# Performance work log

Measured on AMD Instinct MI355X. Metric: run time of the kernel, lower is better.

Reference implementation:

```python
import jax, jax.numpy as jnp
import numpy as np

N_NODES = 50000
N_EDGES = 800000
IN_DIM, HID, OUT = 512, 96, 64


def gcn_conv(x, W, b, src, dst, n_nodes):
    # PyG GCNConv: h = x W; aggregate with sym-normalized adjacency incl. self-loops; add bias.
    h = x @ W  # [N, out]
    ones = jnp.ones_like(dst, dtype=h.dtype)
    deg = jax.ops.segment_sum(ones, dst, num_segments=n_nodes) + 1.0  # +1 for self-loop
    dinv = jax.lax.rsqrt(deg)
    norm = dinv[src] * dinv[dst]  # [E]
    agg = jax.ops.segment_sum(h[src] * norm[:, None], dst, num_segments=n_nodes)
    agg = agg + h * (dinv * dinv)[:, None]  # self-loop messages
    return agg + b


def setup_inputs() -> dict:
    key = jax.random.key(0)
    ks = jax.random.split(key, 12)
    s = 0.05
    x = jax.random.normal(ks[0], (N_NODES, IN_DIM), jnp.float32)
    edge_index = jax.random.randint(ks[1], (2, N_EDGES), 0, N_NODES)
    return {
        "x": x,
        "edge_index": edge_index,
        "W0": jax.random.normal(ks[2], (IN_DIM, HID), jnp.float32) * s,
        "b0": jnp.zeros((HID,), jnp.float32),
        "W1": jax.random.normal(ks[3], (HID, HID), jnp.float32) * s,
        "b1": jnp.zeros((HID,), jnp.float32),
        "W2": jax.random.normal(ks[4], (HID, HID), jnp.float32) * s,
        "b2": jnp.zeros((HID,), jnp.float32),
        "fcW": jax.random.normal(ks[5], (HID, OUT), jnp.float32) * s,
        "fcb": jnp.zeros((OUT,), jnp.float32),
    }


def reference(x, edge_index, W0, b0, W1, b1, W2, b2, fcW, fcb):
    src, dst = edge_index[0], edge_index[1]
    n = x.shape[0]
    # eval mode: dropout is identity; bn=False so no batchnorm
    h = jax.nn.relu(gcn_conv(x, W0, b0, src, dst, n))
    h = jax.nn.relu(gcn_conv(h, W1, b1, src, dst, n))
    h = jax.nn.relu(gcn_conv(h, W2, b2, src, dst, n))
    out = h @ fcW + fcb
    return jnp.squeeze(out)
```

## Files before the change

kernel.cpp:

```cpp
#include <hip/hip_runtime.h>


constexpr int NN   = 50000;
constexpr int NE   = 800000;
constexpr int KIN  = 512;
constexpr int HIDD = 96;
constexpr int ODIM = 64;
constexpr int NBLK = (NN + 255) / 256;

typedef short bf16x8 __attribute__((ext_vector_type(8)));
typedef float f32x4  __attribute__((ext_vector_type(4)));
typedef _Float16 h4  __attribute__((ext_vector_type(4)));

__device__ inline short f2bf(float f) {
    union { float f; unsigned u; } v; v.f = f;
    unsigned r = v.u + 0x7FFFu + ((v.u >> 16) & 1u);
    return (short)(r >> 16);
}
__device__ inline short f2bf_trunc(float f) {
    union { float f; unsigned u; } v; v.f = f;
    return (short)(v.u >> 16);
}
__device__ inline float bf2f(short h) {
    union { unsigned u; float f; } v; v.u = ((unsigned)(unsigned short)h) << 16;
    return v.f;
}

__global__ void zero_int_kernel(int* __restrict__ p, int n) {
    int i = blockIdx.x * blockDim.x + threadIdx.x;
    if (i < n) p[i] = 0;
}

__global__ void hist_kernel(const int* __restrict__ dst, int* __restrict__ deg) {
    int e = blockIdx.x * blockDim.x + threadIdx.x;
    if (e < NE) atomicAdd(&deg[dst[e]], 1);
}

__global__ void scan1_kernel(const int* __restrict__ deg, int* __restrict__ excl,
                             int* __restrict__ partials) {
    __shared__ int tmp[256];
    const int tid = threadIdx.x;
    const int i = blockIdx.x * 256 + tid;
    const int v = (i < NN) ? deg[i] : 0;
    tmp[tid] = v;
    __syncthreads();
#pragma unroll
    for (int off = 1; off < 256; off <<= 1) {
        int t = (tid >= off) ? tmp[tid - off] : 0;
        __syncthreads();
        tmp[tid] += t;
        __syncthreads();
    }
    if (i < NN) excl[i] = tmp[tid] - v;
    if (tid == 255) partials[blockIdx.x] = tmp[tid];
}

__global__ void scan3_kernel(const int* __restrict__ excl, const int* __restrict__ partials,
                             const int* __restrict__ deg, int* __restrict__ rowstart,
                             float* __restrict__ dinv, int* __restrict__ cursor) {
    __shared__ int tmp[256];
    const int tid = threadIdx.x;
    tmp[tid] = (tid < (int)blockIdx.x) ? partials[tid] : 0;
    __syncthreads();
#pragma unroll
    for (int off = 128; off > 0; off >>= 1) {
        if (tid < off) tmp[tid] += tmp[tid + off];
        __syncthreads();
    }
    const int boff = tmp[0];
    const int i = blockIdx.x * 256 + tid;
    if (i < NN) {
        rowstart[i] = excl[i] + boff;
        dinv[i] = 1.0f / sqrtf((float)deg[i] + 1.0f);
        cursor[i] = 0;
    }
}

__global__ void scatter_kernel(const int* __restrict__ src, const int* __restrict__ dst,
                               const int* __restrict__ rowstart, int* __restrict__ cursor,
                               int* __restrict__ csr_src) {
    int e = blockIdx.x * blockDim.x + threadIdx.x;
    if (e < NE) {
        const int d = dst[e];
        const int pos = rowstart[d] + atomicAdd(&cursor[d], 1);
        csr_src[pos] = src[e];
    }
}

__global__ void pack_all(const float* __restrict__ W0, const float* __restrict__ W1,
                         const float* __restrict__ W2, const float* __restrict__ FC,
                         short* __restrict__ w0hi, short* __restrict__ w0lo,
                         short* __restrict__ w1hi, short* __restrict__ w1lo,
                         short* __restrict__ w2hi, short* __restrict__ w2lo,
                         short* __restrict__ fchi, short* __restrict__ fclo) {
    const int idx = blockIdx.x * 256 + threadIdx.x;
    const float* W; short *hi, *lo; int M, li;
    if      (idx < 49152) { W = W0; hi = w0hi; lo = w0lo; M = 96; li = idx; }
    else if (idx < 58368) { W = W1; hi = w1hi; lo = w1lo; M = 96; li = idx - 49152; }
    else if (idx < 67584) { W = W2; hi = w2hi; lo = w2lo; M = 96; li = idx - 58368; }
    else if (idx < 73728) { W = FC; hi = fchi; lo = fclo; M = 64; li = idx - 67584; }
    else return;
    const int CT = M >> 4;
    const int j = li & 7;
    const int lane = (li >> 3) & 63;
    const int t = li >> 9;
    const int ct = t % CT;
    const int kc = t / CT;
    const int k = kc * 32 + (lane >> 4) * 8 + j;
    const int n = ct * 16 + (lane & 15);
    const float w = W[k * M + n];
    const short h = f2bf(w);
    hi[li] = h;
    lo[li] = f2bf_trunc(w - bf2f(h));
}

template <int K>
__launch_bounds__(512, 6)
__global__ void mfma_gemm_f(const float* __restrict__ A, const short* __restrict__ Whi,
                            const short* __restrict__ Wlo, const float* __restrict__ dinv,
                            _Float16* __restrict__ C, int N) {
    constexpr int CT = 6;
    constexpr int KCH = K / 64;
    constexpr int PH  = KCH / 2;
    __shared__ short sHi[4 * 3072];
    __shared__ short sLo[4 * 3072];

    const int tid = threadIdx.x;
    const int lane = tid & 63;
    const int wave = tid >> 6;
    const int rw = wave & 3;
    const int kh = wave >> 2;
    const int q = lane >> 4;
    const int m = lane & 15;
    const int row = blockIdx.x * 64 + rw * 16 + m;
    const int arow = (row < N) ? row : (N - 1);

    f32x4 acc[CT];
#pragma unroll
    for (int c = 0; c < CT; ++c) acc[c] = f32x4{0.f, 0.f, 0.f, 0.f};

    const float* ap = A + (size_t)arow * K + kh * (K / 2) + q * 8;
    float4 a0 = *(const float4*)(ap);
    float4 a1 = *(const float4*)(ap + 4);

#pragma unroll
    for (int p = 0; p < PH; ++p) {
#pragma unroll
        for (int i = 0; i < 3; ++i) {
            const int ci = i * 512 + tid;
            const int slot = ci / 384;
            const int within = ci - slot * 384;
            const int kcg = (slot >> 1) * KCH + p * 2 + (slot & 1);
            const int so = kcg * 3072 + within * 8;
            const int doff = ci * 8;
            *(float4*)(sHi + doff) = *(const float4*)(Whi + so);
            *(float4*)(sLo + doff) = *(const float4*)(Wlo + so);
        }
        __syncthreads();

#pragma unroll
        for (int kc = 0; kc < 2; ++kc) {
            const float af[8] = {a0.x, a0.y, a0.z, a0.w, a1.x, a1.y, a1.z, a1.w};
            bf16x8 ahi, alo;
#pragma unroll
            for (int j = 0; j < 8; ++j) {
                const short h = f2bf(af[j]);
                ahi[j] = h;
                alo[j] = f2bf_trunc(af[j] - bf2f(h));
            }
            if (p * 2 + kc + 1 < KCH) {
                ap += 32;
                a0 = *(const float4*)(ap);
                a1 = *(const float4*)(ap + 4);
            }
            const int slot = kh * 2 + kc;
            const short* hbase = sHi + slot * 3072 + lane * 8;
            const short* lbase = sLo + slot * 3072 + lane * 8;
#pragma unroll
            for (int c = 0; c < CT; ++c) {
                const bf16x8 wh = *(const bf16x8*)(hbase + c * 512);
                const bf16x8 wl = *(const bf16x8*)(lbase + c * 512);
                acc[c] = __builtin_amdgcn_mfma_f32_16x16x32_bf16(ahi, wh, acc[c], 0, 0, 0);
                acc[c] = __builtin_amdgcn_mfma_f32_16x16x32_bf16(alo, wh, acc[c], 0, 0, 0);
                acc[c] = __builtin_amdgcn_mfma_f32_16x16x32_bf16(ahi, wl, acc[c], 0, 0, 0);
            }
        }
        __syncthreads();
    }

    float* sAcc = (float*)sHi;
    if (kh == 1) {
#pragma unroll
        for (int c = 0; c < CT; ++c)
            *(f32x4*)(sAcc + ((rw * 64 + lane) * CT + c) * 4) = acc[c];
    }
    __syncthreads();
    if (kh == 0) {
#pragma unroll
        for (int c = 0; c < CT; ++c) {
            const f32x4 o = *(const f32x4*)(sAcc + ((rw * 64 + lane) * CT + c) * 4);
            acc[c][0] += o[0]; acc[c][1] += o[1]; acc[c][2] += o[2]; acc[c][3] += o[3];
        }
        const int rbase = blockIdx.x * 64 + rw * 16 + q * 4;
#pragma unroll
        for (int r = 0; r < 4; ++r) {
            const int orow = rbase + r;
            if (orow < N) {
                const float s = dinv[orow];
#pragma unroll
                for (int c = 0; c < CT; ++c)
                    C[(size_t)orow * 96 + c * 16 + m] = (_Float16)(acc[c][r] * s);
            }
        }
    }
}

constexpr int APAD = 104;
template <int M, bool FC>
__launch_bounds__(512, 6)
__global__ void fused_gg(const int* __restrict__ rowstart, const int* __restrict__ deg,
                         const int* __restrict__ csr_src, const float* __restrict__ dinv,
                         const h4* __restrict__ hs, const float* __restrict__ gb,
                         const short* __restrict__ Whi, const short* __restrict__ Wlo,
                         const float* __restrict__ bias2,
                         _Float16* __restrict__ Ch, float* __restrict__ Cf, int N) {
    constexpr int CT = M / 16;
    constexpr int CTH = CT / 2;
    __shared__ short sAhi[64 * APAD];
    __shared__ short sAlo[64 * APAD];

    const int tid = threadIdx.x;
    const int nl = tid >> 3;
    const int f8 = tid & 7;
    const int node = blockIdx.x * 64 + nl;
    const bool valid = node < N;

    float acc[12];
#pragma unroll
    for (int i = 0; i < 12; ++i) acc[i] = 0.0f;

    if (valid) {
        const h4* __restrict__ hp = hs + (size_t)node * 24 + f8 * 3;
        {
            const h4 s0 = hp[0], s1 = hp[1], s2 = hp[2];
#pragma unroll
            for (int e = 0; e < 4; ++e) {
                acc[e] += (float)s0[e]; acc[4 + e] += (float)s1[e]; acc[8 + e] += (float)s2[e];
            }
        }
        int j = rowstart[node];
        const int jend = j + deg[node];
        for (; j + 4 <= jend; j += 4) {
            int s[4];
#pragma unroll
            for (int i = 0; i < 4; ++i) s[i] = csr_src[j + i];
            h4 v[4][3];
#pragma unroll
            for (int i = 0; i < 4; ++i) {
                const h4* __restrict__ p = hs + (size_t)s[i] * 24 + f8 * 3;
                v[i][0] = p[0]; v[i][1] = p[1]; v[i][2] = p[2];
            }
#pragma unroll
            for (int i = 0; i < 4; ++i)
#pragma unroll
                for (int e = 0; e < 4; ++e) {
                    acc[e] += (float)v[i][0][e];
                    acc[4 + e] += (float)v[i][1][e];
                    acc[8 + e] += (float)v[i][2][e];
                }
        }
        for (; j < jend; ++j) {
            const h4* __restrict__ p = hs + (size_t)csr_src[j] * 24 + f8 * 3;
            const h4 v0 = p[0], v1 = p[1], v2 = p[2];
#pragma unroll
            for (int e = 0; e < 4; ++e) {
                acc[e] += (float)v0[e]; acc[4 + e] += (float)v1[e]; acc[8 + e] += (float)v2[e];
            }
        }
        const float di = dinv[node];
        short4 hi[3], lo[3];
#pragma unroll
        for (int t = 0; t < 3; ++t) {
#pragma unroll
            for (int e = 0; e < 4; ++e) {
                const float o = fmaxf(fmaf(di, acc[t * 4 + e], gb[f8 * 12 + t * 4 + e]), 0.0f);
                const short h = f2bf(o);
                ((short*)&hi[t])[e] = h;
                ((short*)&lo[t])[e] = f2bf_trunc(o - bf2f(h));
            }
        }
        short* dh = sAhi + nl * APAD + f8 * 12;
        short* dl = sAlo + nl * APAD + f8 * 12;
#pragma unroll
        for (int t = 0; t < 3; ++t) {
            *(short4*)(dh + t * 4) = hi[t];
            *(short4*)(dl + t * 4) = lo[t];
        }
    } else {
        short* dh = sAhi + nl * APAD + f8 * 12;
        short* dl = sAlo + nl * APAD + f8 * 12;
        const short4 z = {0, 0, 0, 0};
#pragma unroll
        for (int t = 0; t < 3; ++t) { *(short4*)(dh + t * 4) = z; *(short4*)(dl + t * 4) = z; }
    }
    __syncthreads();

    const int lane = tid & 63;
    const int wave = tid >> 6;
    const int rw = wave & 3;
    const int c0 = (wave >> 2) * CTH;
    const int q = lane >> 4;
    const int m = lane & 15;

    bf16x8 Ah[3], Al[3];
#pragma unroll
    for (int kc = 0; kc < 3; ++kc) {
        const int off = (rw * 16 + m) * APAD + kc * 32 + q * 8;
        Ah[kc] = *(const bf16x8*)(sAhi + off);
        Al[kc] = *(const bf16x8*)(sAlo + off);
    }

    f32x4 gacc[CTH];
#pragma unroll
    for (int c = 0; c < CTH; ++c) gacc[c] = f32x4{0.f, 0.f, 0.f, 0.f};

#pragma unroll
    for (int kc = 0; kc < 3; ++kc) {
#pragma unroll
        for (int c = 0; c < CTH; ++c) {
            const int fo = ((kc * CT + c0 + c) * 64 + lane) * 8;
            const bf16x8 wh = *(const bf16x8*)(Whi + fo);
            const bf16x8 wl = *(const bf16x8*)(Wlo + fo);
            gacc[c] = __builtin_amdgcn_mfma_f32_16x16x32_bf16(Ah[kc], wh, gacc[c], 0, 0, 0);
            gacc[c] = __builtin_amdgcn_mfma_f32_16x16x32_bf16(Al[kc], wh, gacc[c], 0, 0, 0);
            gacc[c] = __builtin_amdgcn_mfma_f32_16x16x32_bf16(Ah[kc], wl, gacc[c], 0, 0, 0);
        }
    }

    const int rbase = blockIdx.x * 64 + rw * 16 + q * 4;
#pragma unroll
    for (int r = 0; r < 4; ++r) {
        const int orow = rbase + r;
        if (orow < N) {
            if (FC) {
#pragma unroll
                for (int c = 0; c < CTH; ++c)
                    Cf[(size_t)orow * M + (c0 + c) * 16 + m] = gacc[c][r] + bias2[(c0 + c) * 16 + m];
            } else {
                const float s = dinv[orow];
#pragma unroll
                for (int c = 0; c < CTH; ++c)
                    Ch[(size_t)orow * M + (c0 + c) * 16 + m] = (_Float16)(gacc[c][r] * s);
            }
        }
    }
}

extern "C" void kernel_launch(void* const* d_in, const int* in_sizes, int n_in,
                              void* d_out, int out_size, void* d_ws, size_t ws_size,
                              hipStream_t stream) {
    const float* x   = (const float*)d_in[0];
    const int*   ei  = (const int*)d_in[1];
    const float* W0  = (const float*)d_in[2];
    const float* b0  = (const float*)d_in[3];
    const float* W1  = (const float*)d_in[4];
    const float* b1  = (const float*)d_in[5];
    const float* W2  = (const float*)d_in[6];
    const float* b2  = (const float*)d_in[7];
    const float* fcW = (const float*)d_in[8];
    const float* fcb = (const float*)d_in[9];
    float* out = (float*)d_out;

    const int* src = ei;
    const int* dst = ei + NE;

    float* ws = (float*)d_ws;
    float* dinv     = ws;
    int*   deg      = (int*)(ws + 50176);
    int*   excl     = (int*)(ws + 100352);
    int*   cursor   = (int*)(ws + 150528);
    int*   rowstart = (int*)(ws + 200704);
    int*   partials = (int*)(ws + 250880);
    int*   csr_src  = (int*)(ws + 251136);
    short* w0hi = (short*)(ws + 1051392);
    short* w0lo = (short*)(ws + 1075968);
    short* w1hi = (short*)(ws + 1100544);
    short* w1lo = (short*)(ws + 1105152);
    short* w2hi = (short*)(ws + 1109760);
    short* w2lo = (short*)(ws + 1114368);
    short* fchi = (short*)(ws + 1118976);
    short* fclo = (short*)(ws + 1122048);
    _Float16* hsA = (_Float16*)(ws + 1125120);
    _Float16* hsB = (_Float16*)(ws + 3525120);

    dim3 b256(256);
    const int gN = NBLK;
    const int gE = (NE + 255) / 256;
    const int gGem = (NN + 63) / 64;
    const int gPack = (73728 + 255) / 256;

    zero_int_kernel<<<gN, b256, 0, stream>>>(deg, NN);
    hist_kernel<<<gE, b256, 0, stream>>>(dst, deg);
    scan1_kernel<<<gN, b256, 0, stream>>>(deg, excl, partials);
    scan3_kernel<<<gN, b256, 0, stream>>>(excl, partials, deg, rowstart, dinv, cursor);
    scatter_kernel<<<gE, b256, 0, stream>>>(src, dst, rowstart, cursor, csr_src);
    pack_all<<<gPack, b256, 0, stream>>>(W0, W1, W2, fcW, w0hi, w0lo, w1hi, w1lo,
                                         w2hi, w2lo, fchi, fclo);

    mfma_gemm_f<KIN><<<gGem, dim3(512), 0, stream>>>(x, w0hi, w0lo, dinv, hsA, NN);

    fused_gg<HIDD, false><<<gGem, dim3(512), 0, stream>>>(
        rowstart, deg, csr_src, dinv, (const h4*)hsA, b0, w1hi, w1lo, nullptr, hsB, nullptr, NN);

    fused_gg<HIDD, false><<<gGem, dim3(512), 0, stream>>>(
        rowstart, deg, csr_src, dinv, (const h4*)hsB, b1, w2hi, w2lo, nullptr, hsA, nullptr, NN);

    fused_gg<ODIM, true><<<gGem, dim3(512), 0, stream>>>(
        rowstart, deg, csr_src, dinv, (const h4*)hsA, b2, fchi, fclo, fcb, nullptr, out, NN);
}
```

Before: 377.8 us.

## Balance edge aggregation across threads with merge-path split and LDS atomics

Each block's edge range is now split evenly across its 64 thread groups instead of one group per node. Each group accumulates runs of edges that share a destination and flushes them into a shared-memory accumulator with atomics. The local destination index is packed into the high bits of the CSR source entries, and rowstart gets a sentinel entry. This aims to remove load imbalance from varying node degrees, at the cost of LDS atomics, an extra zeroing pass and extra barriers.

```diff
diff --git a/kernel.cpp b/kernel.cpp
--- a/kernel.cpp
+++ b/kernel.cpp
@@ -74,6 +74,7 @@
         dinv[i] = 1.0f / sqrtf((float)deg[i] + 1.0f);
         cursor[i] = 0;
     }
+    if (blockIdx.x == 0 && tid == 0) rowstart[NN] = NE;
 }
 
 __global__ void scatter_kernel(const int* __restrict__ src, const int* __restrict__ dst,
@@ -83,7 +84,7 @@
     if (e < NE) {
         const int d = dst[e];
         const int pos = rowstart[d] + atomicAdd(&cursor[d], 1);
-        csr_src[pos] = src[e];
+        csr_src[pos] = src[e] | ((d & 63) << 20);
     }
 }
 
@@ -216,92 +217,106 @@
 }
 
 constexpr int APAD = 104;
+constexpr int ACCS = 97;
 template <int M, bool FC>
 __launch_bounds__(512, 6)
-__global__ void fused_gg(const int* __restrict__ rowstart, const int* __restrict__ deg,
-                         const int* __restrict__ csr_src, const float* __restrict__ dinv,
-                         const h4* __restrict__ hs, const float* __restrict__ gb,
+__global__ void fused_gg(const int* __restrict__ rowstart, const float* __restrict__ dinv,
+                         const int* __restrict__ csr_src, const h4* __restrict__ hs,
+                         const float* __restrict__ gb,
                          const short* __restrict__ Whi, const short* __restrict__ Wlo,
                          const float* __restrict__ bias2,
                          _Float16* __restrict__ Ch, float* __restrict__ Cf, int N) {
     constexpr int CT = M / 16;
     constexpr int CTH = CT / 2;
-    __shared__ short sAhi[64 * APAD];
-    __shared__ short sAlo[64 * APAD];
+    __shared__ short SMEM[2 * 64 * APAD];
+    float* accf = (float*)SMEM;
+    short* sAhi = SMEM;
+    short* sAlo = SMEM + 64 * APAD;
 
     const int tid = threadIdx.x;
+    const int nb = blockIdx.x * 64;
+
+    for (int i = tid; i < 64 * ACCS; i += 512) accf[i] = 0.0f;
+    __syncthreads();
+
+    {
+        const int e0 = rowstart[nb];
+        const int top = (nb + 64 < N) ? nb + 64 : N;
+        const int T = rowstart[top] - e0;
+        const int g = tid >> 3;
+        const int f8 = tid & 7;
+        const int per = (T + 63) >> 6;
+        int j = g * per;
+        const int jend = (j + per < T) ? (j + per) : T;
+
+        float racc[12];
+#pragma unroll
+        for (int i = 0; i < 12; ++i) racc[i] = 0.f;
+        int curloc = -1;
+        int v = (j < jend) ? csr_src[e0 + j] : 0;
+        while (j < jend) {
+            const int vn = (j + 1 < jend) ? csr_src[e0 + j + 1] : 0;
+            const int s = v & 0xFFFFF;
+            const int loc = v >> 20;
+            if (loc != curloc) {
+                if (curloc >= 0) {
+#pragma unroll
+                    for (int i = 0; i < 12; ++i)
+                        atomicAdd(&accf[curloc * ACCS + f8 * 12 + i], racc[i]);
+                }
+#pragma unroll
+                for (int i = 0; i < 12; ++i) racc[i] = 0.f;
+                curloc = loc;
+            }
+            const h4* __restrict__ p = hs + (size_t)s * 24 + f8 * 3;
+            const h4 p0 = p[0], p1 = p[1], p2 = p[2];
+#pragma unroll
+            for (int e = 0; e < 4; ++e) {
+                racc[e] += (float)p0[e]; racc[4 + e] += (float)p1[e]; racc[8 + e] += (float)p2[e];
+            }
+            v = vn; ++j;
+        }
+        if (curloc >= 0) {
+#pragma unroll
+            for (int i = 0; i < 12; ++i)
+                atomicAdd(&accf[curloc * ACCS + f8 * 12 + i], racc[i]);
+        }
+    }
+    __syncthreads();
+
     const int nl = tid >> 3;
-    const int f8 = tid & 7;
-    const int node = blockIdx.x * 64 + nl;
-    const bool valid = node < N;
-
-    float acc[12];
-#pragma unroll
-    for (int i = 0; i < 12; ++i) acc[i] = 0.0f;
-
-    if (valid) {
-        const h4* __restrict__ hp = hs + (size_t)node * 24 + f8 * 3;
-        {
-            const h4 s0 = hp[0], s1 = hp[1], s2 = hp[2];
-#pragma unroll
-            for (int e = 0; e < 4; ++e) {
-                acc[e] += (float)s0[e]; acc[4 + e] += (float)s1[e]; acc[8 + e] += (float)s2[e];
-            }
-        }
-        int j = rowstart[node];
-        const int jend = j + deg[node];
-        for (; j + 4 <= jend; j += 4) {
-            int s[4];
-#pragma unroll
-            for (int i = 0; i < 4; ++i) s[i] = csr_src[j + i];
-            h4 v[4][3];
-#pragma unroll
-            for (int i = 0; i < 4; ++i) {
-                const h4* __restrict__ p = hs + (size_t)s[i] * 24 + f8 * 3;
-                v[i][0] = p[0]; v[i][1] = p[1]; v[i][2] = p[2];
-            }
-#pragma unroll
-            for (int i = 0; i < 4; ++i)
-#pragma unroll
-                for (int e = 0; e < 4; ++e) {
-                    acc[e] += (float)v[i][0][e];
-                    acc[4 + e] += (float)v[i][1][e];
-                    acc[8 + e] += (float)v[i][2][e];
-                }
-        }
-        for (; j < jend; ++j) {
-            const h4* __restrict__ p = hs + (size_t)csr_src[j] * 24 + f8 * 3;
-            const h4 v0 = p[0], v1 = p[1], v2 = p[2];
-#pragma unroll
-            for (int e = 0; e < 4; ++e) {
-                acc[e] += (float)v0[e]; acc[4 + e] += (float)v1[e]; acc[8 + e] += (float)v2[e];
-            }
-        }
+    const int fc8 = tid & 7;
+    const int node = nb + nl;
+    short hi[12], lo[12];
+    if (node < N) {
+        const h4* __restrict__ hp = hs + (size_t)node * 24 + fc8 * 3;
+        const h4 s0 = hp[0], s1 = hp[1], s2 = hp[2];
         const float di = dinv[node];
-        short4 hi[3], lo[3];
-#pragma unroll
-        for (int t = 0; t < 3; ++t) {
-#pragma unroll
-            for (int e = 0; e < 4; ++e) {
-                const float o = fmaxf(fmaf(di, acc[t * 4 + e], gb[f8 * 12 + t * 4 + e]), 0.0f);
-                const short h = f2bf(o);
-                ((short*)&hi[t])[e] = h;
-                ((short*)&lo[t])[e] = f2bf_trunc(o - bf2f(h));
-            }
-        }
-        short* dh = sAhi + nl * APAD + f8 * 12;
-        short* dl = sAlo + nl * APAD + f8 * 12;
-#pragma unroll
-        for (int t = 0; t < 3; ++t) {
-            *(short4*)(dh + t * 4) = hi[t];
-            *(short4*)(dl + t * 4) = lo[t];
+        float a[12];
+#pragma unroll
+        for (int i = 0; i < 12; ++i) a[i] = accf[nl * ACCS + fc8 * 12 + i];
+#pragma unroll
+        for (int e = 0; e < 4; ++e) {
+            a[e] += (float)s0[e]; a[4 + e] += (float)s1[e]; a[8 + e] += (float)s2[e];
+        }
+#pragma unroll
+        for (int i = 0; i < 12; ++i) {
+            const float o = fmaxf(fmaf(di, a[i], gb[fc8 * 12 + i]), 0.0f);
+            hi[i] = f2bf(o);
+            lo[i] = f2bf_trunc(o - bf2f(hi[i]));
         }
     } else {
-        short* dh = sAhi + nl * APAD + f8 * 12;
-        short* dl = sAlo + nl * APAD + f8 * 12;
-        const short4 z = {0, 0, 0, 0};
-#pragma unroll
-        for (int t = 0; t < 3; ++t) { *(short4*)(dh + t * 4) = z; *(short4*)(dl + t * 4) = z; }
+#pragma unroll
+        for (int i = 0; i < 12; ++i) { hi[i] = 0; lo[i] = 0; }
+    }
+    __syncthreads();
+
+    short* dh = sAhi + nl * APAD + fc8 * 12;
+    short* dl = sAlo + nl * APAD + fc8 * 12;
+#pragma unroll
+    for (int t = 0; t < 3; ++t) {
+        *(short4*)(dh + t * 4) = make_short4(hi[4 * t], hi[4 * t + 1], hi[4 * t + 2], hi[4 * t + 3]);
+        *(short4*)(dl + t * 4) = make_short4(lo[4 * t], lo[4 * t + 1], lo[4 * t + 2], lo[4 * t + 3]);
     }
     __syncthreads();
 
@@ -337,7 +352,7 @@
         }
     }
 
-    const int rbase = blockIdx.x * 64 + rw * 16 + q * 4;
+    const int rbase = nb + rw * 16 + q * 4;
 #pragma unroll
     for (int r = 0; r < 4; ++r) {
         const int orow = rbase + r;
@@ -410,11 +425,11 @@
     mfma_gemm_f<KIN><<<gGem, dim3(512), 0, stream>>>(x, w0hi, w0lo, dinv, hsA, NN);
 
     fused_gg<HIDD, false><<<gGem, dim3(512), 0, stream>>>(
-        rowstart, deg, csr_src, dinv, (const h4*)hsA, b0, w1hi, w1lo, nullptr, hsB, nullptr, NN);
+        rowstart, dinv, csr_src, (const h4*)hsA, b0, w1hi, w1lo, nullptr, hsB, nullptr, NN);
 
     fused_gg<HIDD, false><<<gGem, dim3(512), 0, stream>>>(
-        rowstart, deg, csr_src, dinv, (const h4*)hsB, b1, w2hi, w2lo, nullptr, hsA, nullptr, NN);
+        rowstart, dinv, csr_src, (const h4*)hsB, b1, w2hi, w2lo, nullptr, hsA, nullptr, NN);
 
     fused_gg<ODIM, true><<<gGem, dim3(512), 0, stream>>>(
-        rowstart, deg, csr_src, dinv, (const h4*)hsA, b2, fchi, fclo, fcb, nullptr, out, NN);
-}
+        rowstart, dinv, csr_src, (const h4*)hsA, b2, fchi, fclo, fcb, nullptr, out, NN);
+}
```

After: 487.5 us. 1.29x slower.
